# Kernel optimization log

Hardware: AMD Instinct MI355X
Metric: run time of the kernel (lower is better)

Reference implementation:

```python
import jax, jax.numpy as jnp
import numpy as np
from jax.scipy.special import erf

# module constants (init kwargs)
BOX = 128
RES = 1.0
EPS_IN = 6.5
EPS_OUT = 79.0
ION_SIZE = 1.0
WAT_SIZE = 1.4
ASIGMA = 2.0
KAPPA02 = 0.106
CHARGE_CONV = 7046.52
WR = 8       # splat window radius in voxels ~ ceil(R_max + probe + d*asigma)
N_ITER = 30  # Jacobi iterations for the linearized PB solve


def setup_inputs():
    key = jax.random.key(0)
    kc, kq, kr, kn = jax.random.split(key, 4)
    B, N = 2, 1024
    lo, hi = 0.2 * BOX * RES, 0.8 * BOX * RES
    coords = jax.random.uniform(kc, (B, 3 * N), dtype=jnp.float32, minval=lo, maxval=hi)
    charges = 0.5 * jax.random.normal(kq, (B, N), dtype=jnp.float32)
    radii = jax.random.uniform(kr, (B, N), dtype=jnp.float32, minval=1.0, maxval=2.0)
    assigned_params = jnp.stack([charges, radii], axis=-1)  # [B,N,2] = (charge, radius)
    num_atoms = jax.random.randint(kn, (B,), N // 2, N + 1, dtype=jnp.int32)
    return {"coords": coords, "assigned_params": assigned_params, "num_atoms": num_atoms}


def _flat_scatter_add(vals, idx, B):
    # idx [...,3] int32 clipped voxel indices; vals same leading shape; batched scatter-add
    flat = (idx[..., 0] * BOX + idx[..., 1]) * BOX + idx[..., 2]
    flat = flat + (jnp.arange(B, dtype=jnp.int32) * (BOX ** 3)).reshape((B,) + (1,) * (flat.ndim - 1))
    acc = jnp.zeros((B * BOX ** 3,), vals.dtype).at[flat.reshape(-1)].add(vals.reshape(-1))
    return acc.reshape(B, BOX, BOX, BOX)


def _eps_channel(xyz, radii, atom_mask, offset, extra_r):
    # rho_sum(x) = prod_atoms (1 - smoothed_indicator); accumulated in log space via scatter-add
    o = jnp.arange(-WR, WR + 1, dtype=jnp.int32)
    offs = jnp.stack(jnp.meshgrid(o, o, o, indexing="ij"), axis=-1).reshape(-1, 3)  # [W3,3]
    idx0 = jnp.round(xyz / RES - offset).astype(jnp.int32)            # [B,N,3]
    idx = idx0[:, :, None, :] + offs[None, None]                      # [B,N,W3,3]
    pos = (idx.astype(xyz.dtype) + offset) * RES
    r = jnp.sqrt(jnp.sum((pos - xyz[:, :, None, :]) ** 2, axis=-1) + 1e-12)
    rho = 0.5 * (1.0 - erf((r - (radii[:, :, None] + extra_r)) / ASIGMA))
    logv = jnp.log1p(-jnp.clip(rho, 0.0, 1.0 - 1e-6))
    inb = jnp.all((idx >= 0) & (idx < BOX), axis=-1)
    logv = jnp.where(inb & atom_mask[:, :, None], logv, 0.0)
    acc = _flat_scatter_add(logv, jnp.clip(idx, 0, BOX - 1), xyz.shape[0])
    return jnp.exp(acc)


def _coords2q(xyz, charges, atom_mask):
    # trilinear charge spreading onto the voxel grid
    g = xyz / RES
    i0 = jnp.floor(g).astype(jnp.int32)
    f = g - i0.astype(g.dtype)
    c = jnp.stack(jnp.meshgrid(*([jnp.arange(2)] * 3), indexing="ij"), -1).reshape(-1, 3)  # [8,3]
    idx = i0[:, :, None, :] + c[None, None]                           # [B,N,8,3]
    w = jnp.prod(jnp.where(c[None, None].astype(bool), f[:, :, None, :], 1.0 - f[:, :, None, :]), axis=-1)
    vals = w * charges[:, :, None]
    inb = jnp.all((idx >= 0) & (idx < BOX), axis=-1)
    vals = jnp.where(inb & atom_mask[:, :, None], vals, 0.0)
    return _flat_scatter_add(vals, jnp.clip(idx, 0, BOX - 1), xyz.shape[0])


def _shift(a, axis, step):
    # out[i] = a[i+step], zero padded (Dirichlet phi=0 boundary)
    pad = [(0, 0)] * a.ndim
    sl = [slice(None)] * a.ndim
    if step == 1:
        pad[axis] = (0, 1); sl[axis] = slice(1, None)
    else:
        pad[axis] = (1, 0); sl[axis] = slice(0, -1)
    return jnp.pad(a, pad)[tuple(sl)]


def _qeps2phi(q, eps):
    # Jacobi iteration for div(eps grad phi) - kappa02*lambda*phi = -q on staggered eps grids
    ex, ey, ez, lmbd = eps[:, 0], eps[:, 1], eps[:, 2], eps[:, 3]
    exm, eym, ezm = _shift(ex, 1, -1), _shift(ey, 2, -1), _shift(ez, 3, -1)
    denom = ex + exm + ey + eym + ez + ezm + KAPPA02 * lmbd * RES ** 2
    rhs = q * RES ** 2
    def body(_, phi):
        num = (ex * _shift(phi, 1, 1) + exm * _shift(phi, 1, -1)
               + ey * _shift(phi, 2, 1) + eym * _shift(phi, 2, -1)
               + ez * _shift(phi, 3, 1) + ezm * _shift(phi, 3, -1) + rhs)
        return num / denom
    return jax.lax.fori_loop(0, N_ITER, body, jnp.zeros_like(q))


def reference(coords, assigned_params, num_atoms):
    B = coords.shape[0]
    N = coords.shape[1] // 3
    xyz = coords.reshape(B, N, 3)
    atom_mask = jnp.arange(N)[None, :] < num_atoms[:, None]
    charges, radii = assigned_params[..., 0], assigned_params[..., 1]
    # channels 0..2: face-staggered eps grids (water probe); channel 3: ion accessibility
    specs = [((0.5, 0.0, 0.0), WAT_SIZE), ((0.0, 0.5, 0.0), WAT_SIZE),
             ((0.0, 0.0, 0.5), WAT_SIZE), ((0.0, 0.0, 0.0), ION_SIZE)]
    rho = jnp.stack([_eps_channel(xyz, radii, atom_mask, jnp.asarray(off, xyz.dtype), er)
                     for off, er in specs], axis=1)  # [B,4,S,S,S]
    eps = jnp.concatenate([(1.0 - rho[:, :3]) * (EPS_IN - EPS_OUT) + EPS_OUT,
                           (1.0 - rho[:, 3:4])], axis=1)
    q = _coords2q(xyz, charges, atom_mask) * CHARGE_CONV
    phi = _qeps2phi(q, eps)
    return (q, eps, phi)
```

## Files before the change

kernel.cpp:

```cpp
#include <hip/hip_runtime.h>
#include <math.h>

#define BOX 128
#define MCELLS (BOX*BOX*BOX)
#define TABN 512
#define SATN 256
typedef unsigned short u16;

__device__ __forceinline__ float bf2f(u16 h) {
  union { unsigned u; float f; } c; c.u = ((unsigned)h) << 16; return c.f;
}
__device__ __forceinline__ u16 f2bf(float f) {
  union { float f; unsigned u; } c; c.f = f;
  unsigned r = c.u + 0x7FFF + ((c.u >> 16) & 1);
  return (u16)(r >> 16);
}
__device__ __forceinline__ unsigned pk2(float a, float b) {
  return (unsigned)f2bf(a) | ((unsigned)f2bf(b) << 16);
}
__device__ __forceinline__ float plo(unsigned p) {
  union { unsigned u; float f; } c; c.u = p << 16; return c.f;
}
__device__ __forceinline__ float phh(unsigned p) {
  union { unsigned u; float f; } c; c.u = p & 0xFFFF0000u; return c.f;
}
__device__ __forceinline__ void up8(uint4 p, float* o) {
  o[0] = plo(p.x); o[1] = phh(p.x); o[2] = plo(p.y); o[3] = phh(p.y);
  o[4] = plo(p.z); o[5] = phh(p.z); o[6] = plo(p.w); o[7] = phh(p.w);
}
__device__ __forceinline__ uint4 pk8(const float* o) {
  return make_uint4(pk2(o[0], o[1]), pk2(o[2], o[3]),
                    pk2(o[4], o[5]), pk2(o[6], o[7]));
}

__device__ __forceinline__ float f_exact(float u) {
  float au = fabsf(u);
  float tt = __builtin_amdgcn_rcpf(fmaf(0.3275911f, au, 1.0f));
  float poly = tt * fmaf(tt, fmaf(tt, fmaf(tt, fmaf(tt, 1.061405429f,
                   -1.453152027f), 1.421413741f), -0.284496736f),
                   0.254829592f);
  float e = fmaf(-poly, __expf(-u * u), 1.0f);
  float erfu = (u < 0.0f) ? -e : e;
  float s = fmaf(0.5f, erfu, 0.5f);
  s = fminf(fmaxf(s, 1e-6f), 1.0f);
  return __logf(s);
}

__device__ __forceinline__ float tlook(const float2* __restrict__ ftab,
                                       float r2, float aoff, float hidu) {
  float r = sqrtf(r2 + 1e-12f);
  float t = fmaf(r, hidu, aoff);
  t = fminf(fmaxf(t, 0.0f), 511.75f);
  int j = (int)t;
  float fr = t - (float)j;
  float2 e = ftab[j];
  return fmaf(fr, e.y, e.x);
}

__global__ __launch_bounds__(256) void eps_gather_kernel(
    const float* __restrict__ coords, const float* __restrict__ params,
    const int* __restrict__ num_atoms, float* __restrict__ eps_out, int N) {
  __shared__ float4 sat[SATN];
  __shared__ float2 ftab[TABN];
  __shared__ int scnt;

  const int xt = blockIdx.x, yt = blockIdx.y;
  const int bz = blockIdx.z;
  const int b = bz >> 4, zt = bz & 15;
  const int tid = threadIdx.x;

  const float u0 = -1.8f;
  const float du = (2.2f - u0) / (float)TABN;
  const float inv_du = (float)TABN / (2.2f - u0);
  const float hidu = 0.5f * inv_du;

  if (tid == 0) scnt = 0;
  __syncthreads();

  const float lox = (float)(xt * 8), hix = lox + 7.5f;
  const float loy = (float)(yt * 8), hiy = loy + 7.5f;
  const float loz = (float)(zt * 8), hiz = loz + 7.5f;

  const int na = num_atoms[b];
  for (int a = tid; a < N; a += 256) {
    if (a < na) {
      float ax = coords[(size_t)b * 3 * N + a * 3 + 0];
      float ay = coords[(size_t)b * 3 * N + a * 3 + 1];
      float az = coords[(size_t)b * 3 * N + a * 3 + 2];
      float rad = params[((size_t)b * N + a) * 2 + 1];
      float cx = fminf(fmaxf(ax, lox), hix);
      float cy = fminf(fmaxf(ay, loy), hiy);
      float cz = fminf(fmaxf(az, loz), hiz);
      float ddx = ax - cx, ddy = ay - cy, ddz = az - cz;
      float cut = rad + 5.85f;
      if (ddx * ddx + ddy * ddy + ddz * ddz < cut * cut) {
        int s = atomicAdd(&scnt, 1);
        if (s < SATN) sat[s] = make_float4(ax, ay, az, rad);
      }
    }
  }
  __syncthreads();
  const int cnt = min(scnt, SATN);

  const int zq = tid & 3, yy = (tid >> 2) & 7, xx = tid >> 5;
  const int xi = xt * 8 + xx, yi = yt * 8 + yy, zi = zt * 8 + zq * 2;
  const int v = (xi << 14) + (yi << 7) + zi;
  const size_t eb = (size_t)b * 4 * MCELLS;

  if (cnt == 0) {
    *(float2*)(eps_out + eb + 0 * MCELLS + v) = make_float2(79.0f, 79.0f);
    *(float2*)(eps_out + eb + 1 * MCELLS + v) = make_float2(79.0f, 79.0f);
    *(float2*)(eps_out + eb + 2 * MCELLS + v) = make_float2(79.0f, 79.0f);
    *(float2*)(eps_out + eb + (size_t)3 * MCELLS + v) = make_float2(0.0f, 0.0f);
    return;
  }

  for (int j = tid; j < TABN; j += 256) {
    float uj = fmaf(du, (float)j, u0);
    float f0 = f_exact(uj);
    float f1 = f_exact(uj + du);
    ftab[j] = (j == TABN - 1) ? make_float2(0.0f, 0.0f)
                              : make_float2(f0, f1 - f0);
  }
  __syncthreads();

  const float xf = (float)xi, yf = (float)yi, zf = (float)zi;
  float acc[4][2] = {{0.f, 0.f}, {0.f, 0.f}, {0.f, 0.f}, {0.f, 0.f}};

  for (int j = 0; j < cnt; ++j) {
    float4 A = sat[j];
    float dx = xf - A.x, dy = yf - A.y, dzb = zf - A.z;
    float Rw = A.w + 1.4f;
    float cw = Rw + 4.4f;
    float cw2 = cw * cw;
    float aW = (1.8f - 0.5f * Rw) * inv_du;
    float aI = aW + 0.2f * inv_du;

    float dx2 = dx * dx, dxh = dx + 0.5f, dxh2 = dxh * dxh;
    float dy2 = dy * dy, dyh = dy + 0.5f, dyh2 = dyh * dyh;
    float mdx = fminf(dx2, dxh2);
    float mdy = fminf(dy2, dyh2);
    float zhi = dzb + 1.5f;
    float mdz = (dzb > 0.f) ? dzb * dzb : (zhi < 0.f ? zhi * zhi : 0.f);
    if (mdx + mdy + mdz >= cw2) continue;

#pragma unroll
    for (int k = 0; k < 2; ++k) {
      float dzv = dzb + (float)k;
      float dz2 = dzv * dzv, dzh = dzv + 0.5f, dzh2 = dzh * dzh;
      acc[0][k] += tlook(ftab, dxh2 + dy2 + dz2, aW, hidu);
      acc[1][k] += tlook(ftab, dx2 + dyh2 + dz2, aW, hidu);
      acc[2][k] += tlook(ftab, dx2 + dy2 + dzh2, aW, hidu);
      acc[3][k] += tlook(ftab, dx2 + dy2 + dz2, aI, hidu);
    }
  }

#pragma unroll
  for (int ch = 0; ch < 4; ++ch) {
    float e0 = __expf(acc[ch][0]), e1 = __expf(acc[ch][1]);
    float2 o = (ch < 3)
        ? make_float2(fmaf(72.5f, e0, 6.5f), fmaf(72.5f, e1, 6.5f))
        : make_float2(1.0f - e0, 1.0f - e1);
    *(float2*)(eps_out + eb + (size_t)ch * MCELLS + v) = o;
  }
}

__global__ __launch_bounds__(256) void q_scatter_kernel(
    const float* __restrict__ coords, const float* __restrict__ params,
    const int* __restrict__ num_atoms, float* __restrict__ q, int N, int B) {
  int t = blockIdx.x * blockDim.x + threadIdx.x;
  if (t >= B * N) return;
  int b = t / N, atom = t % N;
  if (atom >= num_atoms[b]) return;

  const float x = coords[(size_t)b * 3 * N + atom * 3 + 0];
  const float y = coords[(size_t)b * 3 * N + atom * 3 + 1];
  const float z = coords[(size_t)b * 3 * N + atom * 3 + 2];
  const float c = params[((size_t)b * N + atom) * 2 + 0] * 7046.52f;

  float fx0 = floorf(x), fy0 = floorf(y), fz0 = floorf(z);
  int ix = (int)fx0, iy = (int)fy0, iz = (int)fz0;
  float fx = x - fx0, fy = y - fy0, fz = z - fz0;

  float* __restrict__ g = q + (size_t)b * MCELLS;
  for (int k = 0; k < 8; ++k) {
    int cx = (k >> 2) & 1, cy = (k >> 1) & 1, cz = k & 1;
    int jx = ix + cx, jy = iy + cy, jz = iz + cz;
    if ((unsigned)jx >= (unsigned)BOX || (unsigned)jy >= (unsigned)BOX ||
        (unsigned)jz >= (unsigned)BOX) continue;
    float w = (cx ? fx : 1.0f - fx) * (cy ? fy : 1.0f - fy) *
              (cz ? fz : 1.0f - fz);
    atomicAdd(&g[(jx * BOX + jy) * BOX + jz], w * c);
  }
}

__global__ __launch_bounds__(256) void prep8_kernel(
    const float* __restrict__ eps, const float* __restrict__ q,
    u16* __restrict__ exb, u16* __restrict__ eyb, u16* __restrict__ ezb,
    u16* __restrict__ rdn, u16* __restrict__ rq2, u16* __restrict__ phiA,
    unsigned char* __restrict__ pure, int B) {
  const int per_b = MCELLS / 8;
  int t = blockIdx.x * 256 + threadIdx.x;
  if (t >= B * per_b) return;
  int b = t >> 18;
  int r = t & (per_b - 1);
  int zg = r & 15, y = (r >> 4) & 127, x = r >> 11;
  int z0 = zg << 3;
  int v = (x << 14) | (y << 7) | z0;
  size_t cell = (size_t)b * MCELLS + v;

  const float* ex = eps + (size_t)(b * 4 + 0) * MCELLS;
  const float* ey = eps + (size_t)(b * 4 + 1) * MCELLS;
  const float* ez = eps + (size_t)(b * 4 + 2) * MCELLS;
  const float* lm = eps + (size_t)(b * 4 + 3) * MCELLS;

  float exA[8], eyA[8], ezA9[9], lA[8], qA[8], xmA[8], ymA[8];
  *(float4*)(exA)     = *(const float4*)(ex + v);
  *(float4*)(exA + 4) = *(const float4*)(ex + v + 4);
  *(float4*)(eyA)     = *(const float4*)(ey + v);
  *(float4*)(eyA + 4) = *(const float4*)(ey + v + 4);
  *(float4*)(ezA9 + 1) = *(const float4*)(ez + v);
  *(float4*)(ezA9 + 5) = *(const float4*)(ez + v + 4);
  ezA9[0] = (z0 > 0) ? ez[v - 1] : 0.0f;
  *(float4*)(lA)     = *(const float4*)(lm + v);
  *(float4*)(lA + 4) = *(const float4*)(lm + v + 4);
  *(float4*)(qA)     = *(const float4*)(q + cell);
  *(float4*)(qA + 4) = *(const float4*)(q + cell + 4);
  if (x > 0) {
    *(float4*)(xmA)     = *(const float4*)(ex + v - 16384);
    *(float4*)(xmA + 4) = *(const float4*)(ex + v - 16384 + 4);
  } else {
#pragma unroll
    for (int i = 0; i < 8; ++i) xmA[i] = 0.0f;
  }
  if (y > 0) {
    *(float4*)(ymA)     = *(const float4*)(ey + v - 128);
    *(float4*)(ymA + 4) = *(const float4*)(ey + v - 128 + 4);
  } else {
#pragma unroll
    for (int i = 0; i < 8; ++i) ymA[i] = 0.0f;
  }

  float rdA[8], rqA[8];
  bool pu = true;
#pragma unroll
  for (int i = 0; i < 8; ++i) {
    float den = exA[i] + xmA[i] + eyA[i] + ymA[i] + ezA9[i + 1] + ezA9[i] +
                0.106f * lA[i];
    rdA[i] = __builtin_amdgcn_rcpf(den);
    rqA[i] = qA[i] * rdA[i];
    pu &= (exA[i] == 79.0f) & (eyA[i] == 79.0f) & (ezA9[i + 1] == 79.0f) &
          (lA[i] == 0.0f) & (qA[i] == 0.0f);
  }
  *(uint4*)(exb + cell) = pk8(exA);
  *(uint4*)(eyb + cell) = pk8(eyA);
  *(uint4*)(ezb + cell) = pk8(ezA9 + 1);
  *(uint4*)(rdn + cell) = pk8(rdA);
  uint4 rqp = pk8(rqA);
  *(uint4*)(rq2 + cell) = rqp;
  *(uint4*)(phiA + cell) = rqp;

  unsigned long long bal = __ballot(pu);
  int lane = threadIdx.x & 63;
  if ((lane & 15) == 0) {
    unsigned m = (unsigned)((bal >> (lane & 48)) & 0xFFFFull);
    pure[((size_t)b << 14) + (x << 7) + y] = (m == 0xFFFFu) ? 1 : 0;
  }
}

__global__ __launch_bounds__(256) void flag_kernel(
    const unsigned char* __restrict__ pure, unsigned char* __restrict__ flags,
    int B) {
  int t = blockIdx.x * 256 + threadIdx.x;
  if (t >= B * 128 * 32) return;
  int b = t >> 12;
  int r = t & 4095;
  int x = r >> 5, yq = r & 31;
  unsigned char f = 0;
  if (x > 0 && x < 127 && yq > 0 && yq < 31) {
    const unsigned char* P = pure + ((size_t)b << 14);
    bool ok = true;
    int y0 = yq << 2;
    for (int dx = -1; dx <= 1; ++dx)
      for (int yy = y0 - 1; yy <= y0 + 4; ++yy)
        ok &= (P[(x + dx) * 128 + yy] != 0);
    f = ok ? 1 : 0;
  }
  flags[t] = f;
}

__device__ __forceinline__ void stage8(
    const u16* __restrict__ sp, int cst, int c0, int z0, size_t cell,
    int gx, int gy, bool bulk,
    const u16* __restrict__ exb, const u16* __restrict__ eyb,
    const u16* __restrict__ ezb, const u16* __restrict__ rdn,
    const u16* __restrict__ rq2, float* o) {
  const u16* pc0 = sp + (c0 << 7) + z0;
  uint4 pc = *(const uint4*)pc0;
  u16 zmu = (z0 > 0)   ? pc0[-1] : (u16)0;
  u16 zpu = (z0 < 120) ? pc0[8]  : (u16)0;
  uint4 xp = *(const uint4*)(pc0 + (cst << 7));
  uint4 xm = *(const uint4*)(pc0 - (cst << 7));
  uint4 yp = *(const uint4*)(pc0 + 128);
  uint4 ym = *(const uint4*)(pc0 - 128);

  float pz[10];
  pz[0] = bf2f(zmu); up8(pc, pz + 1); pz[9] = bf2f(zpu);
  float xpA[8], xmA[8], ypA[8], ymA[8];
  up8(xp, xpA); up8(xm, xmA); up8(yp, ypA); up8(ym, ymA);

  if (bulk) {
    float rdc  = bf2f(f2bf(__builtin_amdgcn_rcpf(474.0f)));
    float rdc0 = bf2f(f2bf(__builtin_amdgcn_rcpf(395.0f)));
#pragma unroll
    for (int i = 0; i < 8; ++i) {
      float s = xpA[i] + xmA[i] + ypA[i] + ymA[i] + pz[i] + pz[i + 2];
      float rd = (z0 + i == 0) ? rdc0 : rdc;
      o[i] = rd * (79.0f * s);
    }
  } else {
    const uint4 z4 = make_uint4(0, 0, 0, 0);
    uint4 ec  = *(const uint4*)(exb + cell);
    uint4 em  = (gx > 0) ? *(const uint4*)(exb + cell - 16384) : z4;
    uint4 yc  = *(const uint4*)(eyb + cell);
    uint4 ym4 = (gy > 0) ? *(const uint4*)(eyb + cell - 128) : z4;
    uint4 zc  = *(const uint4*)(ezb + cell);
    u16 ezm0  = (z0 > 0) ? ezb[cell - 1] : (u16)0;
    uint4 rd4 = *(const uint4*)(rdn + cell);
    uint4 rq4 = *(const uint4*)(rq2 + cell);
    float exA[8], exmA[8], eyA[8], eymA[8], ezA[9], rdA[8], rqA[8];
    up8(ec, exA); up8(em, exmA); up8(yc, eyA); up8(ym4, eymA);
    ezA[0] = bf2f(ezm0); up8(zc, ezA + 1);
    up8(rd4, rdA); up8(rq4, rqA);
#pragma unroll
    for (int i = 0; i < 8; ++i) {
      float num = exA[i] * xpA[i];
      num = fmaf(exmA[i], xmA[i], num);
      num = fmaf(eyA[i],  ypA[i], num);
      num = fmaf(eymA[i], ymA[i], num);
      num = fmaf(ezA[i + 1], pz[i + 2], num);
      num = fmaf(ezA[i],     pz[i],     num);
      o[i] = fmaf(rdA[i], num, rqA[i]);
    }
  }
}

__global__ __launch_bounds__(256) void fused2_kernel(
    const u16* __restrict__ pin, u16* __restrict__ pout,
    const u16* __restrict__ exb, const u16* __restrict__ eyb,
    const u16* __restrict__ ezb, const u16* __restrict__ rdn,
    const u16* __restrict__ rq2, const unsigned char* __restrict__ pure) {
  __shared__ u16 s0[12 * 8 * 128];
  __shared__ u16 s1[10 * 6 * 128];
  __shared__ unsigned char sbulk[96];

  const int flat = blockIdx.x;
  const int xcd = flat & 7;
  const int idx = flat >> 3;
  const int x0 = ((xcd << 1) | (idx & 1)) * 8;
  const int rem = idx >> 1;
  const int y0 = (rem & 31) * 4;
  const int b = rem >> 5;

  const int tid = threadIdx.x;
  const size_t bbase = (size_t)b << 21;
  const uint4 z4 = make_uint4(0, 0, 0, 0);

  if (tid < 96) {
    int cx = tid >> 3, cy = tid & 7;
    int gx = x0 - 2 + cx, gy = y0 - 2 + cy;
    bool ok = false;
    if (gx >= 1 && gx <= 126 && gy >= 1 && gy <= 126) {
      const unsigned char* P = pure + ((size_t)b << 14);
      ok = P[(gx << 7) + gy] && P[((gx - 1) << 7) + gy] &&
           P[((gx + 1) << 7) + gy] && P[(gx << 7) + gy - 1] &&
           P[(gx << 7) + gy + 1];
    }
    sbulk[tid] = ok ? 1 : 0;
  }

  for (int i = tid; i < 96 * 16; i += 256) {
    int col = i >> 4, zc = i & 15;
    int cx = col >> 3, cy = col & 7;
    int gx = x0 - 2 + cx, gy = y0 - 2 + cy;
    uint4 vv = z4;
    if ((unsigned)gx < 128u && (unsigned)gy < 128u)
      vv = *(const uint4*)(pin + (bbase | (gx << 14) | (gy << 7) | (zc << 3)));
    ((uint4*)s0)[(col << 4) + zc] = vv;
  }
  __syncthreads();

  for (int u = tid; u < 60 * 16; u += 256) {
    int col = u >> 4, zc = u & 15, zz = zc << 3;
    int cx = col / 6, cy = col - cx * 6;
    int gx = x0 - 1 + cx, gy = y0 - 1 + cy;
    uint4* dst = (uint4*)(s1 + (col << 7) + zz);
    if ((unsigned)gx >= 128u || (unsigned)gy >= 128u) { *dst = z4; continue; }
    int c0 = (cx + 1) * 8 + (cy + 1);
    size_t cell = bbase | (gx << 14) | (gy << 7) | zz;
    float o[8];
    stage8(s0, 8, c0, zz, cell, gx, gy, sbulk[c0] != 0,
           exb, eyb, ezb, rdn, rq2, o);
    *dst = pk8(o);
  }
  __syncthreads();

  for (int u = tid; u < 32 * 16; u += 256) {
    int col = u >> 4, zc = u & 15, zz = zc << 3;
    int cx = col >> 2, cy = col & 3;
    int gx = x0 + cx, gy = y0 + cy;
    int c1 = (cx + 1) * 6 + (cy + 1);
    size_t cell = bbase | (gx << 14) | (gy << 7) | zz;
    float o[8];
    stage8(s1, 6, c1, zz, cell, gx, gy,
           sbulk[(cx + 2) * 8 + (cy + 2)] != 0, exb, eyb, ezb, rdn, rq2, o);
    *(uint4*)(pout + cell) = pk8(o);
  }
}

__global__ __launch_bounds__(256) void sweep_final_kernel(
    const u16* __restrict__ pin, float* __restrict__ poutf,
    const u16* __restrict__ exb, const u16* __restrict__ eyb,
    const u16* __restrict__ ezb, const u16* __restrict__ rdn,
    const u16* __restrict__ rq2, const unsigned char* __restrict__ flags,
    int units) {
  int t = blockIdx.x * 256 + threadIdx.x;
  if (t >= units) return;
  int b = t >> 18;
  int r = t & ((1 << 18) - 1);
  int zg = r & 15, y = (r >> 4) & 127, x = r >> 11;
  int z0 = zg << 3;
  int v = (x << 14) | (y << 7) | z0;
  size_t cell = (size_t)b * MCELLS + v;

  const uint4 z4 = make_uint4(0, 0, 0, 0);
  uint4 pc = *(const uint4*)(pin + cell);
  u16 zmu = (z0 > 0)   ? pin[cell - 1] : (u16)0;
  u16 zpu = (z0 < 120) ? pin[cell + 8] : (u16)0;
  uint4 xp = (x < 127) ? *(const uint4*)(pin + cell + 16384) : z4;
  uint4 xm = (x > 0)   ? *(const uint4*)(pin + cell - 16384) : z4;
  uint4 yp = (y < 127) ? *(const uint4*)(pin + cell + 128) : z4;
  uint4 ym = (y > 0)   ? *(const uint4*)(pin + cell - 128) : z4;

  float pz[10];
  pz[0] = bf2f(zmu); up8(pc, pz + 1); pz[9] = bf2f(zpu);
  float xpA[8], xmA[8], ypA[8], ymA[8];
  up8(xp, xpA); up8(xm, xmA); up8(yp, ypA); up8(ym, ymA);

  bool bulk = flags[(b << 12) + (x << 5) + (y >> 2)] != 0;

  float o[8];
  if (bulk) {
    float rdc  = bf2f(f2bf(__builtin_amdgcn_rcpf(474.0f)));
    float rdc0 = bf2f(f2bf(__builtin_amdgcn_rcpf(395.0f)));
#pragma unroll
    for (int i = 0; i < 8; ++i) {
      float s = xpA[i] + xmA[i] + ypA[i] + ymA[i] + pz[i] + pz[i + 2];
      float rd = (z0 + i == 0) ? rdc0 : rdc;
      o[i] = rd * (79.0f * s);
    }
  } else {
    uint4 ec  = *(const uint4*)(exb + cell);
    uint4 em  = (x > 0) ? *(const uint4*)(exb + cell - 16384) : z4;
    uint4 yc  = *(const uint4*)(eyb + cell);
    uint4 ym4 = (y > 0) ? *(const uint4*)(eyb + cell - 128) : z4;
    uint4 zc  = *(const uint4*)(ezb + cell);
    u16 ezm0  = (z0 > 0) ? ezb[cell - 1] : (u16)0;
    uint4 rd4 = *(const uint4*)(rdn + cell);
    uint4 rq4 = *(const uint4*)(rq2 + cell);
    float exA[8], exmA[8], eyA[8], eymA[8], ezA[9], rdA[8], rqA[8];
    up8(ec, exA); up8(em, exmA); up8(yc, eyA); up8(ym4, eymA);
    ezA[0] = bf2f(ezm0); up8(zc, ezA + 1);
    up8(rd4, rdA); up8(rq4, rqA);
#pragma unroll
    for (int i = 0; i < 8; ++i) {
      float num = exA[i] * xpA[i];
      num = fmaf(exmA[i], xmA[i], num);
      num = fmaf(eyA[i],  ypA[i], num);
      num = fmaf(eymA[i], ymA[i], num);
      num = fmaf(ezA[i + 1], pz[i + 2], num);
      num = fmaf(ezA[i],     pz[i],     num);
      o[i] = fmaf(rdA[i], num, rqA[i]);
    }
  }
  *(float4*)(poutf + cell)     = make_float4(o[0], o[1], o[2], o[3]);
  *(float4*)(poutf + cell + 4) = make_float4(o[4], o[5], o[6], o[7]);
}

__global__ __launch_bounds__(256) void jacobi_kernel(
    const float* __restrict__ phi_in, float* __restrict__ phi_out,
    const float* __restrict__ eps, const float* __restrict__ rhs, int B) {
  int i = blockIdx.x * blockDim.x + threadIdx.x;
  if (i >= B * MCELLS) return;
  int b = i >> 21;
  int v = i & (MCELLS - 1);
  int z = v & 127, y = (v >> 7) & 127, x = v >> 14;

  const float* ex = eps + (size_t)(b * 4 + 0) * MCELLS;
  const float* ey = eps + (size_t)(b * 4 + 1) * MCELLS;
  const float* ez = eps + (size_t)(b * 4 + 2) * MCELLS;
  const float* lm = eps + (size_t)(b * 4 + 3) * MCELLS;
  const float* p  = phi_in + (size_t)b * MCELLS;

  float exc = ex[v], eyc = ey[v], ezc = ez[v];
  float exm = (x > 0) ? ex[v - BOX * BOX] : 0.0f;
  float eym = (y > 0) ? ey[v - BOX]       : 0.0f;
  float ezm = (z > 0) ? ez[v - 1]         : 0.0f;

  float num = rhs[i];
  num += (x < BOX - 1) ? exc * p[v + BOX * BOX] : 0.0f;
  num += (x > 0)       ? exm * p[v - BOX * BOX] : 0.0f;
  num += (y < BOX - 1) ? eyc * p[v + BOX]       : 0.0f;
  num += (y > 0)       ? eym * p[v - BOX]       : 0.0f;
  num += (z < BOX - 1) ? ezc * p[v + 1]         : 0.0f;
  num += (z > 0)       ? ezm * p[v - 1]         : 0.0f;

  float den = exc + exm + eyc + eym + ezc + ezm + 0.106f * lm[v];
  phi_out[i] = num / den;
}

extern "C" void kernel_launch(void* const* d_in, const int* in_sizes, int n_in,
                              void* d_out, int out_size, void* d_ws,
                              size_t ws_size, hipStream_t stream) {
  const float* coords    = (const float*)d_in[0];
  const float* params    = (const float*)d_in[1];
  const int*   num_atoms = (const int*)d_in[2];

  const int B = in_sizes[2];
  const int N = in_sizes[1] / (2 * B);

  float* out = (float*)d_out;
  float* q   = out;
  float* eps = out + (size_t)B * MCELLS;
  float* phi = out + (size_t)B * MCELLS * 5;

  const size_t BM = (size_t)B * MCELLS;
  u16* phiA = (u16*)d_ws;
  u16* phiB = phiA + BM;
  u16* exb  = phiB + BM;
  u16* eyb  = exb + BM;
  u16* ezb  = eyb + BM;
  u16* rdn  = ezb + BM;
  u16* rq2  = rdn + BM;
  unsigned char* pureb = (unsigned char*)(rq2 + BM);
  unsigned char* flags = pureb + (size_t)B * 16384;
  const size_t need = BM * 14 + (size_t)B * (16384 + 4096);

  const bool fast = (ws_size >= need);

  hipMemsetAsync(q, 0, sizeof(float) * BM, stream);

  eps_gather_kernel<<<dim3(16, 16, 16 * B), 256, 0, stream>>>(
      coords, params, num_atoms, eps, N);
  q_scatter_kernel<<<(B * N + 255) / 256, 256, 0, stream>>>(
      coords, params, num_atoms, q, N, B);

  if (fast) {
    const int pblocks = B * 1024;
    prep8_kernel<<<pblocks, 256, 0, stream>>>(eps, q, exb, eyb, ezb, rdn, rq2,
                                              phiA, pureb, B);
    flag_kernel<<<(B * 4096 + 255) / 256, 256, 0, stream>>>(pureb, flags, B);

    u16* pa = phiA;
    u16* pb = phiB;
    for (int k = 0; k < 14; ++k) {
      fused2_kernel<<<512 * B, 256, 0, stream>>>(
          pa, pb, exb, eyb, ezb, rdn, rq2, pureb);
      u16* tmp = pa; pa = pb; pb = tmp;
    }
    const int units = B * (MCELLS / 8);
    sweep_final_kernel<<<(units + 255) / 256, 256, 0, stream>>>(
        pa, phi, exb, eyb, ezb, rdn, rq2, flags, units);
  } else {
    hipMemsetAsync(phi, 0, sizeof(float) * BM, stream);
    float* pa = phi;
    float* pb = (float*)d_ws;
    int total = (int)BM;
    for (int it = 0; it < 30; ++it) {
      jacobi_kernel<<<(total + 255) / 256, 256, 0, stream>>>(pa, pb, eps, q, B);
      float* tmp = pa; pa = pb; pb = tmp;
    }
  }
}
```

Baseline: 506.8 us.

## Software-pipeline coefficient loads in fused Jacobi kernel and precompute bulk flags

Restructures the two-step Jacobi kernel so the halo tile is loaded straight into LDS with global_load_lds, and per-cell coefficient loads are issued one iteration ahead in registers, overlapping them with stencil math. The per-block bulk-flag computation moves into a separate precomputed bxy kernel, and occupancy is hinted with launch_bounds(256,4). The eps gather kernel also precomputes per-atom cutoff and table offsets in shared memory and uses a raw sqrt intrinsic. This adds register pressure from the double-buffered loads, one extra kernel, and a zero buffer used for out-of-range LDS loads.

Result: slower. 743.3 us (+46.7%).

```diff
diff --git a/kernel.cpp b/kernel.cpp
--- a/kernel.cpp
+++ b/kernel.cpp
@@ -31,6 +31,12 @@
 __device__ __forceinline__ uint4 pk8(const float* o) {
   return make_uint4(pk2(o[0], o[1]), pk2(o[2], o[3]),
                     pk2(o[4], o[5]), pk2(o[6], o[7]));
+}
+
+__device__ __forceinline__ void gload_lds16(const u16* g, u16* l) {
+  __builtin_amdgcn_global_load_lds(
+      (const __attribute__((address_space(1))) unsigned int*)(g),
+      (__attribute__((address_space(3))) unsigned int*)(l), 16, 0, 0);
 }
 
 __device__ __forceinline__ float f_exact(float u) {
@@ -46,9 +52,9 @@
   return __logf(s);
 }
 
-__device__ __forceinline__ float tlook(const float2* __restrict__ ftab,
-                                       float r2, float aoff, float hidu) {
-  float r = sqrtf(r2 + 1e-12f);
+__device__ __forceinline__ float tlookf(const float2* __restrict__ ftab,
+                                        float r2, float aoff, float hidu) {
+  float r = __builtin_amdgcn_sqrtf(r2);
   float t = fmaf(r, hidu, aoff);
   t = fminf(fmaxf(t, 0.0f), 511.75f);
   int j = (int)t;
@@ -60,7 +66,8 @@
 __global__ __launch_bounds__(256) void eps_gather_kernel(
     const float* __restrict__ coords, const float* __restrict__ params,
     const int* __restrict__ num_atoms, float* __restrict__ eps_out, int N) {
-  __shared__ float4 sat[SATN];
+  __shared__ float4 satA[SATN];
+  __shared__ float  satW[SATN];
   __shared__ float2 ftab[TABN];
   __shared__ int scnt;
 
@@ -73,6 +80,7 @@
   const float du = (2.2f - u0) / (float)TABN;
   const float inv_du = (float)TABN / (2.2f - u0);
   const float hidu = 0.5f * inv_du;
+  const float dAI = 0.2f * inv_du;
 
   if (tid == 0) scnt = 0;
   __syncthreads();
@@ -95,7 +103,12 @@
       float cut = rad + 5.85f;
       if (ddx * ddx + ddy * ddy + ddz * ddz < cut * cut) {
         int s = atomicAdd(&scnt, 1);
-        if (s < SATN) sat[s] = make_float4(ax, ay, az, rad);
+        if (s < SATN) {
+          float Rw = rad + 1.4f;
+          float cw = rad + 5.8f;
+          satA[s] = make_float4(ax, ay, az, cw * cw);
+          satW[s] = (1.8f - 0.5f * Rw) * inv_du;
+        }
       }
     }
   }
@@ -128,13 +141,10 @@
   float acc[4][2] = {{0.f, 0.f}, {0.f, 0.f}, {0.f, 0.f}, {0.f, 0.f}};
 
   for (int j = 0; j < cnt; ++j) {
-    float4 A = sat[j];
+    float4 A = satA[j];
+    float aW = satW[j];
     float dx = xf - A.x, dy = yf - A.y, dzb = zf - A.z;
-    float Rw = A.w + 1.4f;
-    float cw = Rw + 4.4f;
-    float cw2 = cw * cw;
-    float aW = (1.8f - 0.5f * Rw) * inv_du;
-    float aI = aW + 0.2f * inv_du;
+    float cw2 = A.w;
 
     float dx2 = dx * dx, dxh = dx + 0.5f, dxh2 = dxh * dxh;
     float dy2 = dy * dy, dyh = dy + 0.5f, dyh2 = dyh * dyh;
@@ -144,14 +154,16 @@
     float mdz = (dzb > 0.f) ? dzb * dzb : (zhi < 0.f ? zhi * zhi : 0.f);
     if (mdx + mdy + mdz >= cw2) continue;
 
+    float aI = aW + dAI;
+    float sW0 = dxh2 + dy2, sW1 = dx2 + dyh2, sxy = dx2 + dy2;
 #pragma unroll
     for (int k = 0; k < 2; ++k) {
       float dzv = dzb + (float)k;
       float dz2 = dzv * dzv, dzh = dzv + 0.5f, dzh2 = dzh * dzh;
-      acc[0][k] += tlook(ftab, dxh2 + dy2 + dz2, aW, hidu);
-      acc[1][k] += tlook(ftab, dx2 + dyh2 + dz2, aW, hidu);
-      acc[2][k] += tlook(ftab, dx2 + dy2 + dzh2, aW, hidu);
-      acc[3][k] += tlook(ftab, dx2 + dy2 + dz2, aI, hidu);
+      acc[0][k] += tlookf(ftab, sW0 + dz2, aW, hidu);
+      acc[1][k] += tlookf(ftab, sW1 + dz2, aW, hidu);
+      acc[2][k] += tlookf(ftab, sxy + dzh2, aW, hidu);
+      acc[3][k] += tlookf(ftab, sxy + dz2, aI, hidu);
     }
   }
 
@@ -289,12 +301,27 @@
   flags[t] = f;
 }
 
-__device__ __forceinline__ void stage8(
-    const u16* __restrict__ sp, int cst, int c0, int z0, size_t cell,
-    int gx, int gy, bool bulk,
-    const u16* __restrict__ exb, const u16* __restrict__ eyb,
-    const u16* __restrict__ ezb, const u16* __restrict__ rdn,
-    const u16* __restrict__ rq2, float* o) {
+__global__ __launch_bounds__(256) void bulkxy_kernel(
+    const unsigned char* __restrict__ pure, unsigned char* __restrict__ bxy,
+    int B) {
+  int t = blockIdx.x * 256 + threadIdx.x;
+  if (t >= B * 16384) return;
+  int b = t >> 14, r = t & 16383;
+  int x = r >> 7, y = r & 127;
+  unsigned char f = 0;
+  if (x >= 1 && x <= 126 && y >= 1 && y <= 126) {
+    const unsigned char* P = pure + ((size_t)b << 14);
+    f = (unsigned char)(P[(x << 7) + y] & P[((x - 1) << 7) + y] &
+                        P[((x + 1) << 7) + y] & P[(x << 7) + y - 1] &
+                        P[(x << 7) + y + 1]);
+  }
+  bxy[t] = f;
+}
+
+__device__ __forceinline__ void stencil8(
+    const u16* __restrict__ sp, int cst, int c0, int z0, bool bulk,
+    uint4 ec, uint4 em, uint4 yc, uint4 ym4, uint4 zc, unsigned ezm0,
+    uint4 rd4, uint4 rq4, float* o) {
   const u16* pc0 = sp + (c0 << 7) + z0;
   uint4 pc = *(const uint4*)pc0;
   u16 zmu = (z0 > 0)   ? pc0[-1] : (u16)0;
@@ -319,18 +346,9 @@
       o[i] = rd * (79.0f * s);
     }
   } else {
-    const uint4 z4 = make_uint4(0, 0, 0, 0);
-    uint4 ec  = *(const uint4*)(exb + cell);
-    uint4 em  = (gx > 0) ? *(const uint4*)(exb + cell - 16384) : z4;
-    uint4 yc  = *(const uint4*)(eyb + cell);
-    uint4 ym4 = (gy > 0) ? *(const uint4*)(eyb + cell - 128) : z4;
-    uint4 zc  = *(const uint4*)(ezb + cell);
-    u16 ezm0  = (z0 > 0) ? ezb[cell - 1] : (u16)0;
-    uint4 rd4 = *(const uint4*)(rdn + cell);
-    uint4 rq4 = *(const uint4*)(rq2 + cell);
     float exA[8], exmA[8], eyA[8], eymA[8], ezA[9], rdA[8], rqA[8];
     up8(ec, exA); up8(em, exmA); up8(yc, eyA); up8(ym4, eymA);
-    ezA[0] = bf2f(ezm0); up8(zc, ezA + 1);
+    ezA[0] = bf2f((u16)ezm0); up8(zc, ezA + 1);
     up8(rd4, rdA); up8(rq4, rqA);
 #pragma unroll
     for (int i = 0; i < 8; ++i) {
@@ -345,14 +363,14 @@
   }
 }
 
-__global__ __launch_bounds__(256) void fused2_kernel(
+__global__ __launch_bounds__(256, 4) void fused2_kernel(
     const u16* __restrict__ pin, u16* __restrict__ pout,
     const u16* __restrict__ exb, const u16* __restrict__ eyb,
     const u16* __restrict__ ezb, const u16* __restrict__ rdn,
-    const u16* __restrict__ rq2, const unsigned char* __restrict__ pure) {
+    const u16* __restrict__ rq2, const unsigned char* __restrict__ bxy,
+    const u16* __restrict__ zb) {
   __shared__ u16 s0[12 * 8 * 128];
   __shared__ u16 s1[10 * 6 * 128];
-  __shared__ unsigned char sbulk[96];
 
   const int flat = blockIdx.x;
   const int xcd = flat & 7;
@@ -364,58 +382,106 @@
 
   const int tid = threadIdx.x;
   const size_t bbase = (size_t)b << 21;
+  const size_t bofs  = (size_t)b << 14;
   const uint4 z4 = make_uint4(0, 0, 0, 0);
 
-  if (tid < 96) {
-    int cx = tid >> 3, cy = tid & 7;
-    int gx = x0 - 2 + cx, gy = y0 - 2 + cy;
-    bool ok = false;
-    if (gx >= 1 && gx <= 126 && gy >= 1 && gy <= 126) {
-      const unsigned char* P = pure + ((size_t)b << 14);
-      ok = P[(gx << 7) + gy] && P[((gx - 1) << 7) + gy] &&
-           P[((gx + 1) << 7) + gy] && P[(gx << 7) + gy - 1] &&
-           P[(gx << 7) + gy + 1];
-    }
-    sbulk[tid] = ok ? 1 : 0;
-  }
-
-  for (int i = tid; i < 96 * 16; i += 256) {
-    int col = i >> 4, zc = i & 15;
-    int cx = col >> 3, cy = col & 7;
-    int gx = x0 - 2 + cx, gy = y0 - 2 + cy;
-    uint4 vv = z4;
-    if ((unsigned)gx < 128u && (unsigned)gy < 128u)
-      vv = *(const uint4*)(pin + (bbase | (gx << 14) | (gy << 7) | (zc << 3)));
-    ((uint4*)s0)[(col << 4) + zc] = vv;
-  }
-  __syncthreads();
-
-  for (int u = tid; u < 60 * 16; u += 256) {
-    int col = u >> 4, zc = u & 15, zz = zc << 3;
+#pragma unroll
+  for (int j = 0; j < 6; ++j) {
+    int i = tid + (j << 8);
+    int col = i >> 4, zcq = i & 15;
+    int gx = x0 - 2 + (col >> 3), gy = y0 - 2 + (col & 7);
+    const u16* src = (((unsigned)gx < 128u) & ((unsigned)gy < 128u))
+        ? (pin + (bbase | ((size_t)gx << 14) | (gy << 7) | (zcq << 3)))
+        : zb;
+    gload_lds16(src, s0 + ((size_t)i << 3));
+  }
+
+  uint4 Rec[2], Rem[2], Ryc[2], Rym[2], Rzc[2], Rrd[2], Rrq[2];
+  unsigned Rez[2];
+  bool blk1[4], blk2[2];
+
+  auto pre1 = [&](int it, int sl) {
+    int u = tid + (it << 8);
+    if (u >= 960) return;
+    int col = u >> 4, zc16 = u & 15, zz = zc16 << 3;
     int cx = col / 6, cy = col - cx * 6;
     int gx = x0 - 1 + cx, gy = y0 - 1 + cy;
-    uint4* dst = (uint4*)(s1 + (col << 7) + zz);
-    if ((unsigned)gx >= 128u || (unsigned)gy >= 128u) { *dst = z4; continue; }
+    if (((unsigned)gx >= 128u) | ((unsigned)gy >= 128u)) return;
+    bool blk = bxy[bofs + (gx << 7) + gy] != 0;
+    blk1[it] = blk;
+    if (blk) return;
+    size_t cell = bbase | ((size_t)gx << 14) | (size_t)(gy << 7) | (size_t)zz;
+    Rec[sl] = *(const uint4*)(exb + cell);
+    Rem[sl] = (gx > 0) ? *(const uint4*)(exb + cell - 16384) : z4;
+    Ryc[sl] = *(const uint4*)(eyb + cell);
+    Rym[sl] = (gy > 0) ? *(const uint4*)(eyb + cell - 128) : z4;
+    Rzc[sl] = *(const uint4*)(ezb + cell);
+    Rez[sl] = (zz > 0) ? (unsigned)ezb[cell - 1] : 0u;
+    Rrd[sl] = *(const uint4*)(rdn + cell);
+    Rrq[sl] = *(const uint4*)(rq2 + cell);
+  };
+
+  auto use1 = [&](int it, int sl) {
+    int u = tid + (it << 8);
+    if (u >= 960) return;
+    int col = u >> 4, zc16 = u & 15, zz = zc16 << 3;
+    uint4* dst = (uint4*)s1 + ((col << 4) + zc16);
+    int cx = col / 6, cy = col - cx * 6;
+    int gx = x0 - 1 + cx, gy = y0 - 1 + cy;
+    if (((unsigned)gx >= 128u) | ((unsigned)gy >= 128u)) { *dst = z4; return; }
     int c0 = (cx + 1) * 8 + (cy + 1);
-    size_t cell = bbase | (gx << 14) | (gy << 7) | zz;
     float o[8];
-    stage8(s0, 8, c0, zz, cell, gx, gy, sbulk[c0] != 0,
-           exb, eyb, ezb, rdn, rq2, o);
+    stencil8(s0, 8, c0, zz, blk1[it], Rec[sl], Rem[sl], Ryc[sl], Rym[sl],
+             Rzc[sl], Rez[sl], Rrd[sl], Rrq[sl], o);
     *dst = pk8(o);
-  }
-  __syncthreads();
-
-  for (int u = tid; u < 32 * 16; u += 256) {
-    int col = u >> 4, zc = u & 15, zz = zc << 3;
+  };
+
+  auto pre2 = [&](int it, int sl) {
+    int u = tid + (it << 8);
+    int col = u >> 4, zc16 = u & 15, zz = zc16 << 3;
+    int cx = col >> 2, cy = col & 3;
+    int gx = x0 + cx, gy = y0 + cy;
+    bool blk = bxy[bofs + (gx << 7) + gy] != 0;
+    blk2[it] = blk;
+    if (blk) return;
+    size_t cell = bbase | ((size_t)gx << 14) | (size_t)(gy << 7) | (size_t)zz;
+    Rec[sl] = *(const uint4*)(exb + cell);
+    Rem[sl] = (gx > 0) ? *(const uint4*)(exb + cell - 16384) : z4;
+    Ryc[sl] = *(const uint4*)(eyb + cell);
+    Rym[sl] = (gy > 0) ? *(const uint4*)(eyb + cell - 128) : z4;
+    Rzc[sl] = *(const uint4*)(ezb + cell);
+    Rez[sl] = (zz > 0) ? (unsigned)ezb[cell - 1] : 0u;
+    Rrd[sl] = *(const uint4*)(rdn + cell);
+    Rrq[sl] = *(const uint4*)(rq2 + cell);
+  };
+
+  auto use2 = [&](int it, int sl) {
+    int u = tid + (it << 8);
+    int col = u >> 4, zc16 = u & 15, zz = zc16 << 3;
     int cx = col >> 2, cy = col & 3;
     int gx = x0 + cx, gy = y0 + cy;
     int c1 = (cx + 1) * 6 + (cy + 1);
-    size_t cell = bbase | (gx << 14) | (gy << 7) | zz;
+    size_t cell = bbase | ((size_t)gx << 14) | (size_t)(gy << 7) | (size_t)zz;
     float o[8];
-    stage8(s1, 6, c1, zz, cell, gx, gy,
-           sbulk[(cx + 2) * 8 + (cy + 2)] != 0, exb, eyb, ezb, rdn, rq2, o);
+    stencil8(s1, 6, c1, zz, blk2[it], Rec[sl], Rem[sl], Ryc[sl], Rym[sl],
+             Rzc[sl], Rez[sl], Rrd[sl], Rrq[sl], o);
     *(uint4*)(pout + cell) = pk8(o);
-  }
+  };
+
+  pre1(0, 0);
+  __syncthreads();
+  pre1(1, 1);
+  use1(0, 0);
+  pre1(2, 0);
+  use1(1, 1);
+  pre1(3, 1);
+  use1(2, 0);
+  use1(3, 1);
+  pre2(0, 0);
+  __syncthreads();
+  pre2(1, 1);
+  use2(0, 0);
+  use2(1, 1);
 }
 
 __global__ __launch_bounds__(256) void sweep_final_kernel(
@@ -544,7 +610,9 @@
   u16* rq2  = rdn + BM;
   unsigned char* pureb = (unsigned char*)(rq2 + BM);
   unsigned char* flags = pureb + (size_t)B * 16384;
-  const size_t need = BM * 14 + (size_t)B * (16384 + 4096);
+  unsigned char* bxy   = flags + (size_t)B * 4096;
+  u16* zb = (u16*)(bxy + (size_t)B * 16384);
+  const size_t need = BM * 14 + (size_t)B * (16384 + 4096 + 16384) + 64;
 
   const bool fast = (ws_size >= need);
 
@@ -560,12 +628,14 @@
     prep8_kernel<<<pblocks, 256, 0, stream>>>(eps, q, exb, eyb, ezb, rdn, rq2,
                                               phiA, pureb, B);
     flag_kernel<<<(B * 4096 + 255) / 256, 256, 0, stream>>>(pureb, flags, B);
+    bulkxy_kernel<<<(B * 16384 + 255) / 256, 256, 0, stream>>>(pureb, bxy, B);
+    hipMemsetAsync(zb, 0, 64, stream);
 
     u16* pa = phiA;
     u16* pb = phiB;
     for (int k = 0; k < 14; ++k) {
       fused2_kernel<<<512 * B, 256, 0, stream>>>(
-          pa, pb, exb, eyb, ezb, rdn, rq2, pureb);
+          pa, pb, exb, eyb, ezb, rdn, rq2, bxy, zb);
       u16* tmp = pa; pa = pb; pb = tmp;
     }
     const int units = B * (MCELLS / 8);
```
